# Performance work log

Measured on AMD Instinct MI355X. Metric: run time of the kernel, lower is better.

Reference implementation:

```python
import jax, jax.numpy as jnp
import numpy as np

NU, NI, DIN, DOUT, NS, E = 100000, 100000, 128, 128, 5, 500000


def setup_inputs() -> dict:
    key = jax.random.key(0)
    ks = jax.random.split(key, 9)
    scale = 1.0 / np.sqrt(DIN)
    return {
        "user_inputs": jax.random.normal(ks[0], (NU, DIN), jnp.float32),
        "item_inputs": jax.random.normal(ks[1], (NI, DIN), jnp.float32),
        "weight": jax.random.normal(ks[2], (DIN, DOUT, NS), jnp.float32) * scale,
        "u_rows": jax.random.randint(ks[3], (NS, E), 0, NU),
        "u_cols": jax.random.randint(ks[4], (NS, E), 0, NI),
        "u_vals": jax.random.uniform(ks[5], (NS, E), jnp.float32),
        "i_rows": jax.random.randint(ks[6], (NS, E), 0, NI),
        "i_cols": jax.random.randint(ks[7], (NS, E), 0, NU),
        "i_vals": jax.random.uniform(ks[8], (NS, E), jnp.float32),
    }


def _spmm(rows, cols, vals, dense, n_rows):
    # COO sparse [n_rows, n_cols] @ dense [n_cols, d] -> [n_rows, d]
    msgs = vals[:, None] * dense[cols]  # [E, d]
    return jax.ops.segment_sum(msgs, rows, num_segments=n_rows)


def reference(user_inputs, item_inputs, weight, u_rows, u_cols, u_vals, i_rows, i_cols, i_vals):
    n_users = user_inputs.shape[0]
    n_items = item_inputs.shape[0]
    num_support = weight.shape[-1]
    w = jnp.zeros(weight.shape[:2], weight.dtype)
    user_hidden = jnp.zeros((n_users, weight.shape[1]), weight.dtype)
    item_hidden = jnp.zeros((n_items, weight.shape[1]), weight.dtype)
    for i in range(num_support):  # fixed small structural loop (5 rating levels)
        w = w + weight[..., i]            # cumulative weight sum, as in original
        tmp_u = user_inputs @ w           # [NU, DOUT]
        tmp_v = item_inputs @ w           # [NI, DOUT]
        user_hidden = user_hidden + _spmm(u_rows[i], u_cols[i], u_vals[i], tmp_v, n_users)
        item_hidden = item_hidden + _spmm(i_rows[i], i_cols[i], i_vals[i], tmp_u, n_items)
    return jax.nn.relu(user_hidden), jax.nn.relu(item_hidden)
```

## Files before the change

kernel.cpp:

```cpp
#include <hip/hip_runtime.h>

#define R_     100000
#define NSUP   5
#define EDGES  500000
#define D_     128
#define ND     (NSUP * D_)
#define BR     64
#define PPS2   ((R_ + BR - 1) / BR)
#define NBIN1  PPS2
#define CAP2   512

#define EPB    8192
#define BPS    62
#define OROWS  1568

using short8 = __attribute__((ext_vector_type(8))) short;
using f32x4  = __attribute__((ext_vector_type(4))) float;

static __device__ __forceinline__ float bf2f_lo(unsigned p) { return __uint_as_float(p << 16); }
static __device__ __forceinline__ float bf2f_hi(unsigned p) { return __uint_as_float(p & 0xffff0000u); }
static __device__ __forceinline__ unsigned short f2bf(float x) {
    unsigned u = __float_as_uint(x);
    return (unsigned short)((u + 0x7fffu + ((u >> 16) & 1u)) >> 16);
}

__global__ __launch_bounds__(256) void prep_k(const float* __restrict__ user_in,
                                              const float* __restrict__ item_in,
                                              const float* __restrict__ w,
                                              unsigned short* __restrict__ srcb,
                                              unsigned short* __restrict__ bt) {
    int b = blockIdx.x, tid = threadIdx.x;
    if (b < 25000) {
        int side = b / 12500;
        int t = (b - side * 12500) * 256 + tid;
        const float* src = side ? user_in : item_in;
        float4 v = *(const float4*)(src + (size_t)t * 4);
        ushort4 o;
        o.x = f2bf(v.x); o.y = f2bf(v.y); o.z = f2bf(v.z); o.w = f2bf(v.w);
        *(ushort4*)(srcb + (size_t)side * (R_ * D_) + (size_t)t * 4) = o;
    } else {
        int t = (b - 25000) * 256 + tid;
        int o = t / ND;
        int kk = t - o * ND;
        int i = kk >> 7, d = kk & 127;
        float s = 0.f;
        for (int j = 0; j <= i; j++) s += w[(d * D_ + o) * NSUP + j];
        bt[t] = f2bf(s);
    }
}

__global__ __launch_bounds__(512) void place2_k(const int* __restrict__ u_rows,
                                                const int* __restrict__ u_cols,
                                                const float* __restrict__ u_vals,
                                                const int* __restrict__ i_rows,
                                                const int* __restrict__ i_cols,
                                                const float* __restrict__ i_vals,
                                                int* __restrict__ offs2,
                                                uint2* __restrict__ cedge2) {
    __shared__ int   hist[NBIN1];
    __shared__ int   part[512];
    __shared__ uint2 estage[EPB];

    int seg = blockIdx.x / BPS;
    int bb  = blockIdx.x - seg * BPS;
    int side = seg / NSUP;
    int sup  = seg - side * NSUP;
    const int*   rows = side ? i_rows : u_rows;
    const int*   cols = side ? i_cols : u_cols;
    const float* vals = side ? i_vals : u_vals;
    int e0 = bb * EPB;
    int ecnt = EDGES - e0; if (ecnt > EPB) ecnt = EPB;
    size_t gb = (size_t)sup * EDGES + e0;
    int tid = threadIdx.x;

    for (int b = tid; b < NBIN1; b += 512) hist[b] = 0;
    __syncthreads();
    for (int e = tid; e < ecnt; e += 512)
        atomicAdd(&hist[rows[gb + e] >> 6], 1);
    __syncthreads();
    int b0 = tid * 4, s4 = 0;
    if (b0 < NBIN1) {
#pragma unroll
        for (int k = 0; k < 4; k++)
            if (b0 + k < NBIN1) s4 += hist[b0 + k];
    }
    part[tid] = s4;
    __syncthreads();
    for (int off = 1; off < 512; off <<= 1) {
        int u = (tid >= off) ? part[tid - off] : 0;
        __syncthreads();
        part[tid] += u;
        __syncthreads();
    }
    int ex = part[tid] - s4;
    int orow = seg * OROWS;
    if (b0 < NBIN1) {
        int run = ex;
#pragma unroll
        for (int k = 0; k < 4; k++) {
            int b = b0 + k;
            if (b < NBIN1) {
                int c = hist[b];
                offs2[(size_t)(orow + b) * 64 + bb] = run;
                hist[b] = run;
                run += c;
            }
        }
    }
    if (tid == 0) offs2[(size_t)(orow + NBIN1) * 64 + bb] = ecnt;
    __syncthreads();
    for (int e = tid; e < ecnt; e += 512) {
        int r = rows[gb + e];
        int pos = atomicAdd(&hist[r >> 6], 1);
        uint2 E;
        E.x = (unsigned)cols[gb + e] | ((unsigned)(r & 63) << 17);
        E.y = __float_as_uint(vals[gb + e]);
        estage[pos] = E;
    }
    __syncthreads();
    size_t cbase = (size_t)(seg * BPS + bb) * EPB;
    for (int e = tid; e < ecnt; e += 512) cedge2[cbase + e] = estage[e];
}

__global__ __launch_bounds__(256) void fused_k(const int* __restrict__ offs2,
                                               const uint2* __restrict__ cedge2,
                                               const unsigned short* __restrict__ srcb,
                                               const unsigned short* __restrict__ BT,
                                               float* __restrict__ out) {
    __shared__ unsigned short stile[BR * D_];
    __shared__ uint2 eds[CAP2];
    __shared__ int rcnt[BR];
    __shared__ int rsc[BR];
    __shared__ int rstart[BPS + 1];
    __shared__ int ro0[BPS];
    uint2* eraw = (uint2*)&stile[0];

    int side = blockIdx.x / PPS2;
    int bin  = blockIdx.x - side * PPS2;
    const unsigned short* srcbf = srcb + (size_t)side * (R_ * D_);
    float* outp = out + (size_t)side * R_ * D_;

    int tid = threadIdx.x;
    int wid = tid >> 6, lane = tid & 63;
    int g = lane >> 4, l16 = lane & 15;

    f32x4 acc[4][2];
#pragma unroll
    for (int rt = 0; rt < 4; rt++)
#pragma unroll
        for (int nt = 0; nt < 2; nt++)
            acc[rt][nt] = (f32x4){0.f, 0.f, 0.f, 0.f};

    for (int i = 0; i < NSUP; i++) {
        int seg = side * NSUP + i;
        __syncthreads();
        if (wid == 0) {
            int o0v = 0, cnt = 0;
            if (lane < BPS) {
                const int* orow = offs2 + ((size_t)seg * OROWS + bin) * 64;
                o0v = orow[lane];
                cnt = orow[lane + 64] - o0v;
            }
            int s = cnt;
#pragma unroll
            for (int off = 1; off < 64; off <<= 1) {
                int u = __shfl_up(s, off, 64);
                if (lane >= off) s += u;
            }
            if (lane < BPS) { rstart[lane] = s - cnt; ro0[lane] = o0v; }
            if (lane == BPS - 1) rstart[BPS] = s;
        } else if (wid == 1 && lane < BR) {
            rcnt[lane] = 0;
        }
        __syncthreads();
        int n = rstart[BPS]; if (n > CAP2) n = CAP2;
        if (tid < 4 * BPS) {
            int rb = tid >> 2, j0 = tid & 3;
            int rs = rstart[rb];
            int cnt = rstart[rb + 1] - rs;
            const uint2* src = cedge2 + (size_t)(seg * BPS + rb) * EPB + ro0[rb];
            for (int j = j0; j < cnt; j += 4) {
                int pos = rs + j;
                if (pos < CAP2) eraw[pos] = src[j];
            }
        }
        __syncthreads();
        for (int e = tid; e < n; e += 256)
            atomicAdd(&rcnt[(eraw[e].x >> 17) & 63], 1);
        __syncthreads();
        if (wid == 0) {
            int vv = rcnt[lane];
            int s = vv;
#pragma unroll
            for (int off = 1; off < 64; off <<= 1) {
                int u = __shfl_up(s, off, 64);
                if (lane >= off) s += u;
            }
            rsc[lane] = s;
            rcnt[lane] = s - vv;
        }
        __syncthreads();
        for (int e = tid; e < n; e += 256) {
            uint2 E = eraw[e];
            int pos = atomicAdd(&rcnt[(E.x >> 17) & 63], 1);
            eds[pos] = E;
        }
        __syncthreads();

        for (int rq = wid; rq < 16; rq += 4) {
            int r = rq * 4 + g;
            int s0 = r ? rsc[r - 1] : 0;
            int e2 = rsc[r];
            float a0 = 0.f, a1 = 0.f, a2 = 0.f, a3 = 0.f;
            float a4 = 0.f, a5 = 0.f, a6 = 0.f, a7 = 0.f;
            int e = s0;
            for (; e + 3 < e2; e += 4) {
                uint2 E0 = eds[e], E1 = eds[e + 1], E2 = eds[e + 2], E3 = eds[e + 3];
                const uint4 p0 = *(const uint4*)(srcbf + (size_t)(E0.x & 0x1FFFFu) * D_ + l16 * 8);
                const uint4 p1 = *(const uint4*)(srcbf + (size_t)(E1.x & 0x1FFFFu) * D_ + l16 * 8);
                const uint4 p2 = *(const uint4*)(srcbf + (size_t)(E2.x & 0x1FFFFu) * D_ + l16 * 8);
                const uint4 p3 = *(const uint4*)(srcbf + (size_t)(E3.x & 0x1FFFFu) * D_ + l16 * 8);
                float v0 = __uint_as_float(E0.y), v1 = __uint_as_float(E1.y);
                float v2 = __uint_as_float(E2.y), v3 = __uint_as_float(E3.y);
                a0 += v0 * bf2f_lo(p0.x); a1 += v0 * bf2f_hi(p0.x);
                a2 += v0 * bf2f_lo(p0.y); a3 += v0 * bf2f_hi(p0.y);
                a4 += v0 * bf2f_lo(p0.z); a5 += v0 * bf2f_hi(p0.z);
                a6 += v0 * bf2f_lo(p0.w); a7 += v0 * bf2f_hi(p0.w);
                a0 += v1 * bf2f_lo(p1.x); a1 += v1 * bf2f_hi(p1.x);
                a2 += v1 * bf2f_lo(p1.y); a3 += v1 * bf2f_hi(p1.y);
                a4 += v1 * bf2f_lo(p1.z); a5 += v1 * bf2f_hi(p1.z);
                a6 += v1 * bf2f_lo(p1.w); a7 += v1 * bf2f_hi(p1.w);
                a0 += v2 * bf2f_lo(p2.x); a1 += v2 * bf2f_hi(p2.x);
                a2 += v2 * bf2f_lo(p2.y); a3 += v2 * bf2f_hi(p2.y);
                a4 += v2 * bf2f_lo(p2.z); a5 += v2 * bf2f_hi(p2.z);
                a6 += v2 * bf2f_lo(p2.w); a7 += v2 * bf2f_hi(p2.w);
                a0 += v3 * bf2f_lo(p3.x); a1 += v3 * bf2f_hi(p3.x);
                a2 += v3 * bf2f_lo(p3.y); a3 += v3 * bf2f_hi(p3.y);
                a4 += v3 * bf2f_lo(p3.z); a5 += v3 * bf2f_hi(p3.z);
                a6 += v3 * bf2f_lo(p3.w); a7 += v3 * bf2f_hi(p3.w);
            }
            for (; e < e2; e++) {
                uint2 E = eds[e];
                const uint4 pk = *(const uint4*)(srcbf + (size_t)(E.x & 0x1FFFFu) * D_ + l16 * 8);
                float vv = __uint_as_float(E.y);
                a0 += vv * bf2f_lo(pk.x); a1 += vv * bf2f_hi(pk.x);
                a2 += vv * bf2f_lo(pk.y); a3 += vv * bf2f_hi(pk.y);
                a4 += vv * bf2f_lo(pk.z); a5 += vv * bf2f_hi(pk.z);
                a6 += vv * bf2f_lo(pk.w); a7 += vv * bf2f_hi(pk.w);
            }
            uint4 P;
            P.x = ((unsigned)f2bf(a1) << 16) | f2bf(a0);
            P.y = ((unsigned)f2bf(a3) << 16) | f2bf(a2);
            P.z = ((unsigned)f2bf(a5) << 16) | f2bf(a4);
            P.w = ((unsigned)f2bf(a7) << 16) | f2bf(a6);
            int boff = r * 256 + ((l16 * 16) ^ ((r & 7) << 4));
            *(uint4*)((char*)stile + boff) = P;
        }
        __syncthreads();

        const unsigned short* btp = BT + (size_t)i * D_;
#pragma unroll
        for (int cc = 0; cc < 4; cc++) {
            short8 afr[4];
#pragma unroll
            for (int rt = 0; rt < 4; rt++) {
                int row = rt * 16 + l16;
                int boff = row * 256 + ((cc * 64 + g * 16) ^ ((row & 7) << 4));
                afr[rt] = *(const short8*)((const char*)stile + boff);
            }
#pragma unroll
            for (int nt = 0; nt < 2; nt++) {
                short8 b = *(const short8*)(btp + (size_t)(wid * 32 + nt * 16 + l16) * ND
                                            + cc * 32 + g * 8);
#pragma unroll
                for (int rt = 0; rt < 4; rt++)
                    acc[rt][nt] = __builtin_amdgcn_mfma_f32_16x16x32_bf16(afr[rt], b,
                                                                          acc[rt][nt], 0, 0, 0);
            }
        }
    }

#pragma unroll
    for (int nt = 0; nt < 2; nt++) {
#pragma unroll
        for (int rt = 0; rt < 4; rt++) {
#pragma unroll
            for (int rr = 0; rr < 4; rr++) {
                int grow = bin * BR + rt * 16 + g * 4 + rr;
                if (grow < R_) {
                    int col = wid * 32 + nt * 16 + l16;
                    float v = acc[rt][nt][rr];
                    outp[(size_t)grow * D_ + col] = v > 0.f ? v : 0.f;
                }
            }
        }
    }
}

extern "C" void kernel_launch(void* const* d_in, const int* in_sizes, int n_in,
                              void* d_out, int out_size, void* d_ws, size_t ws_size,
                              hipStream_t stream) {
    const float* user_in = (const float*)d_in[0];
    const float* item_in = (const float*)d_in[1];
    const float* weight  = (const float*)d_in[2];
    const int* u_rows = (const int*)d_in[3];
    const int* u_cols = (const int*)d_in[4];
    const float* u_vals = (const float*)d_in[5];
    const int* i_rows = (const int*)d_in[6];
    const int* i_cols = (const int*)d_in[7];
    const float* i_vals = (const float*)d_in[8];
    float* out = (float*)d_out;

    char* ws = (char*)d_ws;
    unsigned short* srcb = (unsigned short*)(ws);
    unsigned short* BT   = (unsigned short*)(ws + 51200000);
    uint2* cedge2        = (uint2*)         (ws + 51363840);
    int*   offs2         = (int*)           (ws + 91996160);

    prep_k<<<25320, 256, 0, stream>>>(user_in, item_in, weight, srcb, BT);
    place2_k<<<10 * BPS, 512, 0, stream>>>(u_rows, u_cols, u_vals,
                                           i_rows, i_cols, i_vals, offs2, cedge2);
    fused_k<<<2 * PPS2, 256, 0, stream>>>(offs2, cedge2, srcb, BT, out);
}
```

Before: 590.7 us.

## Split per-row edge sorting into separate kernel and widen fused block to 512 threads

Moves the per-bin gather and row counting-sort of edges out of the fused gather+MFMA kernel into a new rowsort_k. It writes row-sorted edges and per-row prefix tables to workspace, so the fused kernel only copies the pre-sorted edges into shared memory. The fused kernel now runs 512 threads with 8 waves, each owning 16 output columns, and the gather unroll drops from 4 to 2. This adds a launch and an extra global round trip of the edge list in exchange for more parallelism and fewer barriers in the main kernel.

```diff
diff --git a/kernel.cpp b/kernel.cpp
--- a/kernel.cpp
+++ b/kernel.cpp
@@ -122,18 +122,93 @@
     for (int e = tid; e < ecnt; e += 512) cedge2[cbase + e] = estage[e];
 }
 
-__global__ __launch_bounds__(256) void fused_k(const int* __restrict__ offs2,
-                                               const uint2* __restrict__ cedge2,
-                                               const unsigned short* __restrict__ srcb,
-                                               const unsigned short* __restrict__ BT,
-                                               float* __restrict__ out) {
+__global__ __launch_bounds__(256) void rowsort_k(const int* __restrict__ offs2,
+                                                 const uint2* __restrict__ cedge2,
+                                                 uint2* __restrict__ cedge3,
+                                                 int* __restrict__ rtab) {
+    __shared__ uint2 eraw[CAP2];
+    __shared__ uint2 eds[CAP2];
+    __shared__ int rstart[BPS + 1];
+    __shared__ int ro0[BPS];
+    __shared__ int rcnt[BR];
+    __shared__ int rsc[BR];
+
+    int q = blockIdx.x;
+    int seg = q / PPS2;
+    int bin = q - seg * PPS2;
+    int side = seg / NSUP;
+    int sup  = seg - side * NSUP;
+    int tid = threadIdx.x;
+    int wid = tid >> 6, lane = tid & 63;
+
+    if (wid == 0) {
+        int o0v = 0, cnt = 0;
+        if (lane < BPS) {
+            const int* orow = offs2 + ((size_t)seg * OROWS + bin) * 64;
+            o0v = orow[lane];
+            cnt = orow[64 + lane] - o0v;
+        }
+        int s = cnt;
+#pragma unroll
+        for (int off = 1; off < 64; off <<= 1) {
+            int u = __shfl_up(s, off, 64);
+            if (lane >= off) s += u;
+        }
+        if (lane < BPS) { rstart[lane] = s - cnt; ro0[lane] = o0v; }
+        if (lane == BPS - 1) rstart[BPS] = s;
+    } else if (wid == 1 && lane < BR) {
+        rcnt[lane] = 0;
+    }
+    __syncthreads();
+    int n = rstart[BPS]; if (n > CAP2) n = CAP2;
+    if (tid < 4 * BPS) {
+        int rb = tid >> 2, j0 = tid & 3;
+        int rs = rstart[rb];
+        int cnt = rstart[rb + 1] - rs;
+        const uint2* src = cedge2 + (size_t)(seg * BPS + rb) * EPB + ro0[rb];
+        for (int j = j0; j < cnt; j += 4) {
+            int pos = rs + j;
+            if (pos < CAP2) eraw[pos] = src[j];
+        }
+    }
+    __syncthreads();
+    for (int e = tid; e < n; e += 256)
+        atomicAdd(&rcnt[(eraw[e].x >> 17) & 63], 1);
+    __syncthreads();
+    if (wid == 0) {
+        int vv = rcnt[lane];
+        int s = vv;
+#pragma unroll
+        for (int off = 1; off < 64; off <<= 1) {
+            int u = __shfl_up(s, off, 64);
+            if (lane >= off) s += u;
+        }
+        rsc[lane] = s;
+        rcnt[lane] = s - vv;
+    }
+    __syncthreads();
+    if (tid < BR) {
+        int v = rsc[tid]; if (v > CAP2) v = CAP2;
+        rtab[((size_t)(side * PPS2 + bin)) * (NSUP * BR) + sup * BR + tid] = v;
+    }
+    for (int e = tid; e < n; e += 256) {
+        uint2 E = eraw[e];
+        int pos = atomicAdd(&rcnt[(E.x >> 17) & 63], 1);
+        if (pos < CAP2) eds[pos] = E;
+    }
+    __syncthreads();
+    size_t cb = (size_t)q * CAP2;
+    for (int e = tid; e < n; e += 256) cedge3[cb + e] = eds[e];
+}
+
+__global__ __launch_bounds__(512, 8) void fused_k(const uint2* __restrict__ cedge3,
+                                                  const int* __restrict__ rtab,
+                                                  const unsigned short* __restrict__ srcb,
+                                                  const unsigned short* __restrict__ BT,
+                                                  float* __restrict__ out) {
     __shared__ unsigned short stile[BR * D_];
     __shared__ uint2 eds[CAP2];
-    __shared__ int rcnt[BR];
-    __shared__ int rsc[BR];
-    __shared__ int rstart[BPS + 1];
-    __shared__ int ro0[BPS];
-    uint2* eraw = (uint2*)&stile[0];
+    __shared__ int rsc_all[NSUP * BR];
 
     int side = blockIdx.x / PPS2;
     int bin  = blockIdx.x - side * PPS2;
@@ -144,84 +219,33 @@
     int wid = tid >> 6, lane = tid & 63;
     int g = lane >> 4, l16 = lane & 15;
 
-    f32x4 acc[4][2];
-#pragma unroll
-    for (int rt = 0; rt < 4; rt++)
-#pragma unroll
-        for (int nt = 0; nt < 2; nt++)
-            acc[rt][nt] = (f32x4){0.f, 0.f, 0.f, 0.f};
+    if (tid < NSUP * BR)
+        rsc_all[tid] = rtab[((size_t)(side * PPS2 + bin)) * (NSUP * BR) + tid];
+
+    f32x4 acc[4];
+#pragma unroll
+    for (int rt = 0; rt < 4; rt++) acc[rt] = (f32x4){0.f, 0.f, 0.f, 0.f};
 
     for (int i = 0; i < NSUP; i++) {
         int seg = side * NSUP + i;
         __syncthreads();
-        if (wid == 0) {
-            int o0v = 0, cnt = 0;
-            if (lane < BPS) {
-                const int* orow = offs2 + ((size_t)seg * OROWS + bin) * 64;
-                o0v = orow[lane];
-                cnt = orow[lane + 64] - o0v;
-            }
-            int s = cnt;
-#pragma unroll
-            for (int off = 1; off < 64; off <<= 1) {
-                int u = __shfl_up(s, off, 64);
-                if (lane >= off) s += u;
-            }
-            if (lane < BPS) { rstart[lane] = s - cnt; ro0[lane] = o0v; }
-            if (lane == BPS - 1) rstart[BPS] = s;
-        } else if (wid == 1 && lane < BR) {
-            rcnt[lane] = 0;
-        }
-        __syncthreads();
-        int n = rstart[BPS]; if (n > CAP2) n = CAP2;
-        if (tid < 4 * BPS) {
-            int rb = tid >> 2, j0 = tid & 3;
-            int rs = rstart[rb];
-            int cnt = rstart[rb + 1] - rs;
-            const uint2* src = cedge2 + (size_t)(seg * BPS + rb) * EPB + ro0[rb];
-            for (int j = j0; j < cnt; j += 4) {
-                int pos = rs + j;
-                if (pos < CAP2) eraw[pos] = src[j];
-            }
-        }
-        __syncthreads();
-        for (int e = tid; e < n; e += 256)
-            atomicAdd(&rcnt[(eraw[e].x >> 17) & 63], 1);
-        __syncthreads();
-        if (wid == 0) {
-            int vv = rcnt[lane];
-            int s = vv;
-#pragma unroll
-            for (int off = 1; off < 64; off <<= 1) {
-                int u = __shfl_up(s, off, 64);
-                if (lane >= off) s += u;
-            }
-            rsc[lane] = s;
-            rcnt[lane] = s - vv;
-        }
-        __syncthreads();
-        for (int e = tid; e < n; e += 256) {
-            uint2 E = eraw[e];
-            int pos = atomicAdd(&rcnt[(E.x >> 17) & 63], 1);
-            eds[pos] = E;
-        }
-        __syncthreads();
-
-        for (int rq = wid; rq < 16; rq += 4) {
+        int n = rsc_all[i * BR + 63];
+        const uint2* ebase = cedge3 + (size_t)(seg * PPS2 + bin) * CAP2;
+        for (int e = tid; e < n; e += 512) eds[e] = ebase[e];
+        __syncthreads();
+
+        for (int rq = wid; rq < 16; rq += 8) {
             int r = rq * 4 + g;
-            int s0 = r ? rsc[r - 1] : 0;
-            int e2 = rsc[r];
+            int s0 = r ? rsc_all[i * BR + r - 1] : 0;
+            int e2 = rsc_all[i * BR + r];
             float a0 = 0.f, a1 = 0.f, a2 = 0.f, a3 = 0.f;
             float a4 = 0.f, a5 = 0.f, a6 = 0.f, a7 = 0.f;
             int e = s0;
-            for (; e + 3 < e2; e += 4) {
-                uint2 E0 = eds[e], E1 = eds[e + 1], E2 = eds[e + 2], E3 = eds[e + 3];
+            for (; e + 1 < e2; e += 2) {
+                uint2 E0 = eds[e], E1 = eds[e + 1];
                 const uint4 p0 = *(const uint4*)(srcbf + (size_t)(E0.x & 0x1FFFFu) * D_ + l16 * 8);
                 const uint4 p1 = *(const uint4*)(srcbf + (size_t)(E1.x & 0x1FFFFu) * D_ + l16 * 8);
-                const uint4 p2 = *(const uint4*)(srcbf + (size_t)(E2.x & 0x1FFFFu) * D_ + l16 * 8);
-                const uint4 p3 = *(const uint4*)(srcbf + (size_t)(E3.x & 0x1FFFFu) * D_ + l16 * 8);
                 float v0 = __uint_as_float(E0.y), v1 = __uint_as_float(E1.y);
-                float v2 = __uint_as_float(E2.y), v3 = __uint_as_float(E3.y);
                 a0 += v0 * bf2f_lo(p0.x); a1 += v0 * bf2f_hi(p0.x);
                 a2 += v0 * bf2f_lo(p0.y); a3 += v0 * bf2f_hi(p0.y);
                 a4 += v0 * bf2f_lo(p0.z); a5 += v0 * bf2f_hi(p0.z);
@@ -230,14 +254,6 @@
                 a2 += v1 * bf2f_lo(p1.y); a3 += v1 * bf2f_hi(p1.y);
                 a4 += v1 * bf2f_lo(p1.z); a5 += v1 * bf2f_hi(p1.z);
                 a6 += v1 * bf2f_lo(p1.w); a7 += v1 * bf2f_hi(p1.w);
-                a0 += v2 * bf2f_lo(p2.x); a1 += v2 * bf2f_hi(p2.x);
-                a2 += v2 * bf2f_lo(p2.y); a3 += v2 * bf2f_hi(p2.y);
-                a4 += v2 * bf2f_lo(p2.z); a5 += v2 * bf2f_hi(p2.z);
-                a6 += v2 * bf2f_lo(p2.w); a7 += v2 * bf2f_hi(p2.w);
-                a0 += v3 * bf2f_lo(p3.x); a1 += v3 * bf2f_hi(p3.x);
-                a2 += v3 * bf2f_lo(p3.y); a3 += v3 * bf2f_hi(p3.y);
-                a4 += v3 * bf2f_lo(p3.z); a5 += v3 * bf2f_hi(p3.z);
-                a6 += v3 * bf2f_lo(p3.w); a7 += v3 * bf2f_hi(p3.w);
             }
             for (; e < e2; e++) {
                 uint2 E = eds[e];
@@ -258,40 +274,29 @@
         }
         __syncthreads();
 
-        const unsigned short* btp = BT + (size_t)i * D_;
+        const unsigned short* btp = BT + (size_t)(wid * 16 + l16) * ND + i * D_;
 #pragma unroll
         for (int cc = 0; cc < 4; cc++) {
-            short8 afr[4];
+            short8 b = *(const short8*)(btp + cc * 32 + g * 8);
 #pragma unroll
             for (int rt = 0; rt < 4; rt++) {
                 int row = rt * 16 + l16;
                 int boff = row * 256 + ((cc * 64 + g * 16) ^ ((row & 7) << 4));
-                afr[rt] = *(const short8*)((const char*)stile + boff);
-            }
-#pragma unroll
-            for (int nt = 0; nt < 2; nt++) {
-                short8 b = *(const short8*)(btp + (size_t)(wid * 32 + nt * 16 + l16) * ND
-                                            + cc * 32 + g * 8);
-#pragma unroll
-                for (int rt = 0; rt < 4; rt++)
-                    acc[rt][nt] = __builtin_amdgcn_mfma_f32_16x16x32_bf16(afr[rt], b,
-                                                                          acc[rt][nt], 0, 0, 0);
-            }
-        }
-    }
-
-#pragma unroll
-    for (int nt = 0; nt < 2; nt++) {
-#pragma unroll
-        for (int rt = 0; rt < 4; rt++) {
-#pragma unroll
-            for (int rr = 0; rr < 4; rr++) {
-                int grow = bin * BR + rt * 16 + g * 4 + rr;
-                if (grow < R_) {
-                    int col = wid * 32 + nt * 16 + l16;
-                    float v = acc[rt][nt][rr];
-                    outp[(size_t)grow * D_ + col] = v > 0.f ? v : 0.f;
-                }
+                short8 afr = *(const short8*)((const char*)stile + boff);
+                acc[rt] = __builtin_amdgcn_mfma_f32_16x16x32_bf16(afr, b, acc[rt], 0, 0, 0);
+            }
+        }
+    }
+
+#pragma unroll
+    for (int rt = 0; rt < 4; rt++) {
+#pragma unroll
+        for (int rr = 0; rr < 4; rr++) {
+            int grow = bin * BR + rt * 16 + g * 4 + rr;
+            if (grow < R_) {
+                int col = wid * 16 + l16;
+                float v = acc[rt][rr];
+                outp[(size_t)grow * D_ + col] = v > 0.f ? v : 0.f;
             }
         }
     }
@@ -316,9 +321,12 @@
     unsigned short* BT   = (unsigned short*)(ws + 51200000);
     uint2* cedge2        = (uint2*)         (ws + 51363840);
     int*   offs2         = (int*)           (ws + 91996160);
+    uint2* cedge3        = (uint2*)         (ws + 96010240);
+    int*   rtab          = (int*)           (ws + 160030720);
 
     prep_k<<<25320, 256, 0, stream>>>(user_in, item_in, weight, srcb, BT);
     place2_k<<<10 * BPS, 512, 0, stream>>>(u_rows, u_cols, u_vals,
                                            i_rows, i_cols, i_vals, offs2, cedge2);
-    fused_k<<<2 * PPS2, 256, 0, stream>>>(offs2, cedge2, srcb, BT, out);
-}
+    rowsort_k<<<10 * PPS2, 256, 0, stream>>>(offs2, cedge2, cedge3, rtab);
+    fused_k<<<2 * PPS2, 512, 0, stream>>>(cedge3, rtab, srcb, BT, out);
+}
```

Result: faster. 557.1 us (-5.7%).
